# Optimization experiments

Measured on AMD Instinct MI355X. Metric: run time of the kernel, lower is better.

## Reference

```python
import jax, jax.numpy as jnp
import numpy as np

N_NODES = 20000
D = 512
H = 8
DK = D // H  # 64
L = 2


def _layernorm(x, g, b, eps=1e-5):
    mu = x.mean(-1, keepdims=True)
    var = x.var(-1, keepdims=True)
    return (x - mu) / jnp.sqrt(var + eps) * g + b


def _hgt_layer(h, kw, kb, qw, qb, vw, vb, aw, ab, pri, att_r, msg_r, skip, ln_g, ln_b, src, dst):
    # h: [N, D]
    N = h.shape[0]
    k = (h @ kw.T + kb).reshape(N, H, DK)
    q = (h @ qw.T + qb).reshape(N, H, DK)
    v = (h @ vw.T + vb).reshape(N, H, DK)
    # per-relation bilinear transforms on keys and messages
    k = jnp.einsum('nhi,hij->nhj', k, att_r)
    v = jnp.einsum('nhi,hij->nhj', v, msg_r)
    # per-edge attention scores [E, H]
    t = jnp.einsum('ehd,ehd->eh', k[src], q[dst]) * pri / jnp.sqrt(jnp.float32(DK))
    # edge softmax over incoming edges of each destination node
    mx = jax.ops.segment_max(t, dst, num_segments=N)
    e = jnp.exp(t - mx[dst])
    den = jax.ops.segment_sum(e, dst, num_segments=N)
    att = e / jnp.maximum(den[dst], 1e-9)
    # weighted message aggregation [N, H, DK] -> [N, D]
    msg = v[src] * att[..., None]
    agg = jax.ops.segment_sum(msg, dst, num_segments=N).reshape(N, D)
    trans = jax.nn.gelu(agg) @ aw.T + ab
    alpha = jax.nn.sigmoid(skip)
    out = trans * alpha + h * (1.0 - alpha)
    return _layernorm(out, ln_g, ln_b)


def setup_inputs() -> dict:
    key = jax.random.key(0)
    ks = jax.random.split(key, 16)
    B, E = 8192, 320000
    s = 0.02
    inp = {
        'embeddings': jax.random.normal(ks[0], (B, D), jnp.float32),
        'node_emb': jax.random.normal(ks[1], (N_NODES, D), jnp.float32) * s,
        'adapt_w': jax.random.normal(ks[2], (D, D), jnp.float32) * s,
        'adapt_b': jnp.zeros((D,), jnp.float32),
        'kw': jax.random.normal(ks[3], (L, D, D), jnp.float32) * s,
        'kb': jnp.zeros((L, D), jnp.float32),
        'qw': jax.random.normal(ks[4], (L, D, D), jnp.float32) * s,
        'qb': jnp.zeros((L, D), jnp.float32),
        'vw': jax.random.normal(ks[5], (L, D, D), jnp.float32) * s,
        'vb': jnp.zeros((L, D), jnp.float32),
        'aw': jax.random.normal(ks[6], (L, D, D), jnp.float32) * s,
        'ab': jnp.zeros((L, D), jnp.float32),
        'pri': jnp.ones((L, H), jnp.float32),
        'att_r': jax.random.normal(ks[7], (L, H, DK, DK), jnp.float32) * (1.0 / np.sqrt(DK)),
        'msg_r': jax.random.normal(ks[8], (L, H, DK, DK), jnp.float32) * (1.0 / np.sqrt(DK)),
        'skip': jnp.ones((L,), jnp.float32),
        'ln_g': jnp.ones((L, D), jnp.float32),
        'ln_b': jnp.zeros((L, D), jnp.float32),
        'out_w': jax.random.normal(ks[9], (D, D), jnp.float32) * s,
        'out_b': jnp.zeros((D,), jnp.float32),
        'attn_kernels': jax.random.uniform(ks[10], (D,), jnp.float32),
        'src': jax.random.randint(ks[11], (E,), 0, N_NODES, jnp.int32),
        'dst': jax.random.randint(ks[12], (E,), 0, N_NODES, jnp.int32),
        'n_classes': 10000,
    }
    return inp


def reference(embeddings, node_emb, adapt_w, adapt_b, kw, kb, qw, qb, vw, vb, aw, ab,
              pri, att_r, msg_r, skip, ln_g, ln_b, out_w, out_b, attn_kernels,
              src, dst, n_classes):
    # Hgt encoder over the label graph (single ntype '_N')
    h = jax.nn.gelu(node_emb @ adapt_w.T + adapt_b)
    for l in range(L):
        h = _hgt_layer(h, kw[l], kb[l], qw[l], qb[l], vw[l], vb[l], aw[l], ab[l],
                       pri[l], att_r[l], msg_r[l], skip[l], ln_g[l], ln_b[l], src, dst)
    cls_emb = h @ out_w.T + out_b          # [N, D]
    cls_emb = cls_emb[:n_classes]          # [C, D]  (dropout is identity in eval)
    # logits[b,c] = sum_d embeddings[b,d] * attn_kernels[d] * cls_emb[c,d]
    logits = (embeddings * attn_kernels) @ cls_emb.T
    return logits
```

## Files before the change

kernel.cpp:

```cpp
#include <hip/hip_runtime.h>
#include <hip/hip_bf16.h>

#define D 512
#define H 8
#define NLAYER 2

typedef __attribute__((ext_vector_type(8))) short short8;
typedef __attribute__((ext_vector_type(4))) short short4v;
typedef __attribute__((ext_vector_type(4))) float f32x4;

__device__ __forceinline__ float gelu_f(float x) {
    float x3 = x * x * x;
    return 0.5f * x * (1.0f + tanhf(0.7978845608028654f * (x + 0.044715f * x3)));
}

__device__ __forceinline__ unsigned short f2b(float x) {
    unsigned u = __float_as_uint(x);
    u += 0x7FFF + ((u >> 16) & 1);
    return (unsigned short)(u >> 16);
}
__device__ __forceinline__ float b2f(unsigned short u) {
    return __uint_as_float(((unsigned)u) << 16);
}

__device__ __forceinline__ void gld16(const short* g, short* l) {
    __builtin_amdgcn_global_load_lds(
        (const __attribute__((address_space(1))) void*)g,
        (__attribute__((address_space(3))) void*)l, 16, 0, 0);
}

template <int POSTG, int OUTMODE>
__global__ __launch_bounds__(256) void gemm_bf(
    const short* __restrict__ A, const short* __restrict__ B,
    const float* __restrict__ bias, float* __restrict__ Cf,
    short* __restrict__ Cb, int M, int N, int K) {
    __shared__ __align__(16) short As[2][4096];
    __shared__ __align__(16) short Bs[2][4096];
    const unsigned gx = gridDim.x, gy = gridDim.y;
    const unsigned nwg = gx * gy;
    const unsigned orig = blockIdx.y * gx + blockIdx.x;
    const unsigned q = nwg >> 3, r = nwg & 7;
    const unsigned xcd = orig & 7, sidx = orig >> 3;
    const unsigned swz = (xcd < r ? xcd * (q + 1) : r * (q + 1) + (xcd - r) * q) + sidx;
    const unsigned CH = 8;
    const unsigned chunk = swz / (CH * gx);
    const unsigned rem = swz - chunk * (CH * gx);
    const unsigned nr = min(CH, gy - chunk * CH);
    const unsigned col = rem / nr;
    const unsigned rowin = rem - col * nr;
    const int bm = (int)(chunk * CH + rowin) * 128;
    const int bn = (int)col * 128;

    const int tid = threadIdx.x;
    const int lane = tid & 63;
    const int wave = tid >> 6;
    const int wm = (wave >> 1) * 64, wn = (wave & 1) * 64;
    const int lr16 = lane & 15;
    const int lk8 = (lane >> 4) * 8;

    const int trow = tid >> 2;
    const int tchk = (tid & 3) * 8;
    const short* a0 = A + (size_t)min(bm + trow, M - 1) * K + tchk;
    const short* a1 = A + (size_t)min(bm + 64 + trow, M - 1) * K + tchk;
    const short* b0 = B + (size_t)min(bn + trow, N - 1) * K + tchk;
    const short* b1 = B + (size_t)min(bn + 64 + trow, N - 1) * K + tchk;

    auto stage = [&](int buf, int k0) {
        gld16(a0 + k0, &As[buf][tid * 8]);
        gld16(a1 + k0, &As[buf][2048 + tid * 8]);
        gld16(b0 + k0, &Bs[buf][tid * 8]);
        gld16(b1 + k0, &Bs[buf][2048 + tid * 8]);
    };

    f32x4 acc[4][4];
#pragma unroll
    for (int i = 0; i < 4; ++i)
#pragma unroll
        for (int j = 0; j < 4; ++j) acc[i][j] = (f32x4){0.f, 0.f, 0.f, 0.f};

    stage(0, 0);
    int cur = 0;
    for (int k0 = 0; k0 < K; k0 += 32) {
        __syncthreads();
        if (k0 + 32 < K) stage(cur ^ 1, k0 + 32);

        short8 af[4], bfr[4];
#pragma unroll
        for (int mi = 0; mi < 4; ++mi)
            af[mi] = *(const short8*)&As[cur][(wm + mi * 16 + lr16) * 32 + lk8];
#pragma unroll
        for (int ni = 0; ni < 4; ++ni)
            bfr[ni] = *(const short8*)&Bs[cur][(wn + ni * 16 + lr16) * 32 + lk8];
#pragma unroll
        for (int mi = 0; mi < 4; ++mi)
#pragma unroll
            for (int ni = 0; ni < 4; ++ni)
                acc[mi][ni] = __builtin_amdgcn_mfma_f32_16x16x32_bf16(
                    af[mi], bfr[ni], acc[mi][ni], 0, 0, 0);
        cur ^= 1;
    }

#pragma unroll
    for (int mi = 0; mi < 4; ++mi) {
        int row0 = bm + wm + mi * 16 + (lane >> 4) * 4;
#pragma unroll
        for (int ni = 0; ni < 4; ++ni) {
            int col2 = bn + wn + ni * 16 + lr16;
            if (col2 < N) {
                float bsv = bias ? bias[col2] : 0.0f;
#pragma unroll
                for (int rr2 = 0; rr2 < 4; ++rr2) {
                    int row = row0 + rr2;
                    if (row < M) {
                        float v = acc[mi][ni][rr2] + bsv;
                        if (POSTG) v = gelu_f(v);
                        if (OUTMODE != 1) Cf[(size_t)row * N + col2] = v;
                        if (OUTMODE != 0) Cb[(size_t)row * N + col2] = (short)f2b(v);
                    }
                }
            }
        }
    }
}

__global__ void cvt_b16(const float* __restrict__ in, short* __restrict__ out, int n8) {
    int i = blockIdx.x * 256 + threadIdx.x;
    if (i >= n8) return;
    float4 a = ((const float4*)in)[i * 2];
    float4 b = ((const float4*)in)[i * 2 + 1];
    short8 o;
    o[0] = f2b(a.x); o[1] = f2b(a.y); o[2] = f2b(a.z); o[3] = f2b(a.w);
    o[4] = f2b(b.x); o[5] = f2b(b.y); o[6] = f2b(b.z); o[7] = f2b(b.w);
    *(short8*)(out + (size_t)i * 8) = o;
}

__global__ void cp_f32(const float* __restrict__ in, float* __restrict__ out, int n) {
    int i = blockIdx.x * 256 + threadIdx.x;
    if (i < n) out[i] = in[i];
}

__global__ __launch_bounds__(256) void fuse_w(
    const float* __restrict__ w, const float* __restrict__ bsrc,
    const float* __restrict__ r, short* __restrict__ fw, float* __restrict__ fb) {
    int h = blockIdx.y;
    int dc = blockIdx.x * 64;
    __shared__ float rs[64][64];
    int tid = threadIdx.x;
    for (int i = tid; i < 4096; i += 256) rs[i >> 6][i & 63] = r[h * 4096 + i];
    __syncthreads();
    for (int rep = 0; rep < 16; ++rep) {
        int o = rep * 256 + tid;
        int j = o >> 6;
        int dd = o & 63;
        float s = 0.0f;
#pragma unroll 8
        for (int i = 0; i < 64; ++i)
            s = fmaf(rs[i][j], w[(size_t)(h * 64 + i) * D + dc + dd], s);
        fw[(size_t)(h * 64 + j) * D + dc + dd] = (short)f2b(s);
    }
    if (blockIdx.x == 0 && tid < 64) {
        float s = 0.0f;
        for (int i = 0; i < 64; ++i) s += bsrc[h * 64 + i] * rs[i][tid];
        fb[h * 64 + tid] = s;
    }
}

__global__ void zero_int(int* __restrict__ p, int n) {
    int i = blockIdx.x * 256 + threadIdx.x;
    if (i < n) p[i] = 0;
}

__global__ void hist_dst(const int* __restrict__ dst, int* __restrict__ cnt, int E) {
    int i = blockIdx.x * 256 + threadIdx.x;
    if (i < E) atomicAdd(&cnt[dst[i]], 1);
}

__global__ __launch_bounds__(1024) void scan_counts(
    const int* __restrict__ cnt, int* __restrict__ offs, int* __restrict__ cursor,
    int n, int E) {
    __shared__ int part[1024];
    int t = threadIdx.x;
    int chunk = (n + 1023) >> 10;
    int lo = t * chunk;
    int hi = min(lo + chunk, n);
    int s = 0;
    for (int i = lo; i < hi; ++i) s += cnt[i];
    part[t] = s;
    __syncthreads();
    for (int off = 1; off < 1024; off <<= 1) {
        int v = (t >= off) ? part[t - off] : 0;
        __syncthreads();
        part[t] += v;
        __syncthreads();
    }
    int base = (t == 0) ? 0 : part[t - 1];
    for (int i = lo; i < hi; ++i) {
        offs[i] = base;
        cursor[i] = base;
        base += cnt[i];
    }
    if (t == 1023) offs[n] = E;
}

__global__ void scatter_edges(const int* __restrict__ src, const int* __restrict__ dst,
                              int* __restrict__ cursor, int* __restrict__ srcs, int E) {
    int i = blockIdx.x * 256 + threadIdx.x;
    if (i < E) {
        int pos = atomicAdd(&cursor[dst[i]], 1);
        srcs[pos] = src[i];
    }
}

__global__ __launch_bounds__(256) void edge_attn(
    const short* __restrict__ kqv, const int* __restrict__ srcs,
    const int* __restrict__ offs, const float* __restrict__ pri,
    short* __restrict__ gg, int NNodes) {
    int n = blockIdx.x * 4 + (threadIdx.x >> 6);
    if (n >= NNodes) return;
    int lane = threadIdx.x & 63;
    int start = offs[n], end = offs[n + 1];

    const short8 qv = *(const short8*)(kqv + (size_t)n * 1536 + 512 + lane * 8);
    float qf[8];
#pragma unroll
    for (int j = 0; j < 8; ++j) qf[j] = b2f((unsigned short)qv[j]);
    const float prih = pri[lane >> 3] * 0.125f;

    float rm0 = -INFINITY, rd0 = 0.0f, rm1 = -INFINITY, rd1 = 0.0f;
    float va0[8], va1[8];
#pragma unroll
    for (int j = 0; j < 8; ++j) { va0[j] = 0.0f; va1[j] = 0.0f; }

    int i = start;
    for (; i + 1 < end; i += 2) {
        int s0 = srcs[i], s1 = srcs[i + 1];
        const short* r0 = kqv + (size_t)s0 * 1536;
        const short* r1 = kqv + (size_t)s1 * 1536;
        short8 k0 = *(const short8*)(r0 + lane * 8);
        short8 v0 = *(const short8*)(r0 + 1024 + lane * 8);
        short8 k1 = *(const short8*)(r1 + lane * 8);
        short8 v1 = *(const short8*)(r1 + 1024 + lane * 8);
        float d0 = 0.0f, d1 = 0.0f;
#pragma unroll
        for (int j = 0; j < 8; ++j) {
            d0 = fmaf(b2f((unsigned short)k0[j]), qf[j], d0);
            d1 = fmaf(b2f((unsigned short)k1[j]), qf[j], d1);
        }
        d0 += __shfl_xor(d0, 1); d1 += __shfl_xor(d1, 1);
        d0 += __shfl_xor(d0, 2); d1 += __shfl_xor(d1, 2);
        d0 += __shfl_xor(d0, 4); d1 += __shfl_xor(d1, 4);
        float t0 = d0 * prih, t1 = d1 * prih;
        float nm0 = fmaxf(rm0, t0), nm1 = fmaxf(rm1, t1);
        float sc0 = expf(rm0 - nm0), sc1 = expf(rm1 - nm1);
        float e0 = expf(t0 - nm0), e1 = expf(t1 - nm1);
        rd0 = rd0 * sc0 + e0; rm0 = nm0;
        rd1 = rd1 * sc1 + e1; rm1 = nm1;
#pragma unroll
        for (int j = 0; j < 8; ++j) {
            va0[j] = fmaf(va0[j], sc0, b2f((unsigned short)v0[j]) * e0);
            va1[j] = fmaf(va1[j], sc1, b2f((unsigned short)v1[j]) * e1);
        }
    }
    if (i < end) {
        int s0 = srcs[i];
        const short* r0 = kqv + (size_t)s0 * 1536;
        short8 k0 = *(const short8*)(r0 + lane * 8);
        short8 v0 = *(const short8*)(r0 + 1024 + lane * 8);
        float d0 = 0.0f;
#pragma unroll
        for (int j = 0; j < 8; ++j) d0 = fmaf(b2f((unsigned short)k0[j]), qf[j], d0);
        d0 += __shfl_xor(d0, 1);
        d0 += __shfl_xor(d0, 2);
        d0 += __shfl_xor(d0, 4);
        float t0 = d0 * prih;
        float nm0 = fmaxf(rm0, t0);
        float sc0 = expf(rm0 - nm0);
        float e0 = expf(t0 - nm0);
        rd0 = rd0 * sc0 + e0; rm0 = nm0;
#pragma unroll
        for (int j = 0; j < 8; ++j)
            va0[j] = fmaf(va0[j], sc0, b2f((unsigned short)v0[j]) * e0);
    }

    float m = fmaxf(fmaxf(rm0, rm1), -3.0e38f);
    float s0 = expf(rm0 - m), s1 = expf(rm1 - m);
    float rden = rd0 * s0 + rd1 * s1;
    float inv = 1.0f / fmaxf(rden, 1e-9f);
    unsigned o[4];
#pragma unroll
    for (int p = 0; p < 4; ++p) {
        float x0 = gelu_f((va0[2 * p] * s0 + va1[2 * p] * s1) * inv);
        float x1 = gelu_f((va0[2 * p + 1] * s0 + va1[2 * p + 1] * s1) * inv);
        o[p] = (unsigned)(unsigned short)f2b(x0) |
               ((unsigned)(unsigned short)f2b(x1) << 16);
    }
    uint4 pack = make_uint4(o[0], o[1], o[2], o[3]);
    *(uint4*)(gg + (size_t)n * D + lane * 8) = pack;
}

__global__ __launch_bounds__(128) void blend_ln(
    const float* __restrict__ trans, const float* __restrict__ hin,
    const float* __restrict__ skip, const float* __restrict__ g,
    const float* __restrict__ b, float* __restrict__ hout,
    short* __restrict__ hb16) {
    int n = blockIdx.x;
    int tid = threadIdx.x;
    float alpha = 1.0f / (1.0f + expf(-skip[0]));
    size_t base = (size_t)n * D + tid * 4;
    float4 t4 = *(const float4*)(trans + base);
    float4 h4 = *(const float4*)(hin + base);
    float o[4];
    o[0] = t4.x * alpha + h4.x * (1.0f - alpha);
    o[1] = t4.y * alpha + h4.y * (1.0f - alpha);
    o[2] = t4.z * alpha + h4.z * (1.0f - alpha);
    o[3] = t4.w * alpha + h4.w * (1.0f - alpha);
    float s = o[0] + o[1] + o[2] + o[3];
    float ss = o[0] * o[0] + o[1] * o[1] + o[2] * o[2] + o[3] * o[3];
    for (int off = 32; off; off >>= 1) {
        s += __shfl_down(s, off);
        ss += __shfl_down(ss, off);
    }
    __shared__ float red[4];
    if ((tid & 63) == 0) { red[tid >> 6] = s; red[2 + (tid >> 6)] = ss; }
    __syncthreads();
    float S = red[0] + red[1];
    float SS = red[2] + red[3];
    float mu = S * (1.0f / 512.0f);
    float var = SS * (1.0f / 512.0f) - mu * mu;
    float inv = rsqrtf(var + 1e-5f);
    int c = tid * 4;
    float4 o4;
    o4.x = (o[0] - mu) * inv * g[c + 0] + b[c + 0];
    o4.y = (o[1] - mu) * inv * g[c + 1] + b[c + 1];
    o4.z = (o[2] - mu) * inv * g[c + 2] + b[c + 2];
    o4.w = (o[3] - mu) * inv * g[c + 3] + b[c + 3];
    *(float4*)(hout + base) = o4;
    short4v hb;
    hb[0] = f2b(o4.x); hb[1] = f2b(o4.y); hb[2] = f2b(o4.z); hb[3] = f2b(o4.w);
    *(short4v*)(hb16 + base) = hb;
}

__global__ void scale_emb_b16(const float* __restrict__ e, const float* __restrict__ ak,
                              short* __restrict__ o, int n8) {
    int i = blockIdx.x * 256 + threadIdx.x;
    if (i >= n8) return;
    float4 a = ((const float4*)e)[i * 2];
    float4 b = ((const float4*)e)[i * 2 + 1];
    int d0 = (i * 8) & (D - 1);
    short8 v;
    v[0] = f2b(a.x * ak[d0 + 0]); v[1] = f2b(a.y * ak[d0 + 1]);
    v[2] = f2b(a.z * ak[d0 + 2]); v[3] = f2b(a.w * ak[d0 + 3]);
    v[4] = f2b(b.x * ak[d0 + 4]); v[5] = f2b(b.y * ak[d0 + 5]);
    v[6] = f2b(b.z * ak[d0 + 6]); v[7] = f2b(b.w * ak[d0 + 7]);
    *(short8*)(o + (size_t)i * 8) = v;
}

extern "C" void kernel_launch(void* const* d_in, const int* in_sizes, int n_in,
                              void* d_out, int out_size, void* d_ws, size_t ws_size,
                              hipStream_t stream) {
    const float* embeddings = (const float*)d_in[0];
    const float* node_emb   = (const float*)d_in[1];
    const float* adapt_w    = (const float*)d_in[2];
    const float* adapt_b    = (const float*)d_in[3];
    const float* kw   = (const float*)d_in[4];
    const float* kb   = (const float*)d_in[5];
    const float* qw   = (const float*)d_in[6];
    const float* qb   = (const float*)d_in[7];
    const float* vw   = (const float*)d_in[8];
    const float* vb   = (const float*)d_in[9];
    const float* aw   = (const float*)d_in[10];
    const float* ab   = (const float*)d_in[11];
    const float* pri  = (const float*)d_in[12];
    const float* att_r = (const float*)d_in[13];
    const float* msg_r = (const float*)d_in[14];
    const float* skip  = (const float*)d_in[15];
    const float* ln_g  = (const float*)d_in[16];
    const float* ln_b  = (const float*)d_in[17];
    const float* out_w = (const float*)d_in[18];
    const float* out_b = (const float*)d_in[19];
    const float* attn_k = (const float*)d_in[20];
    const int* src = (const int*)d_in[21];
    const int* dst = (const int*)d_in[22];

    const int E  = in_sizes[21];
    const int NB = in_sizes[0] / D;
    const int NN = in_sizes[1] / D;
    const int NC = out_size / NB;

    size_t big = (size_t)NN * D;
    float* hbuf = (float*)d_ws;
    float* fb32 = hbuf + big;
    short* hb16 = (short*)(fb32 + big);
    short* gg16 = hb16 + big;
    short* kqv16 = gg16 + big;
    short* w16a = kqv16 + (size_t)NN * 1536;
    short* w16o = w16a + (size_t)D * D;
    short* w16w = w16o + (size_t)D * D;
    short* wcat = w16w + (size_t)D * D;
    float* bcat = (float*)(wcat + (size_t)1536 * D);
    int* offs   = (int*)(bcat + 1536);
    int* cursor = offs + NN + 1;
    int* srcs   = cursor + NN;
    short* cls16 = kqv16;
    short* embs16 = kqv16 + (size_t)NC * D;

    auto ggrid = [](int M, int N) { return dim3((N + 127) / 128, (M + 127) / 128); };
    const int WB = D * D / 8;

    zero_int<<<(NN + 255) / 256, 256, 0, stream>>>(cursor, NN);
    hist_dst<<<(E + 255) / 256, 256, 0, stream>>>(dst, cursor, E);
    scan_counts<<<1, 1024, 0, stream>>>(cursor, offs, cursor, NN, E);
    scatter_edges<<<(E + 255) / 256, 256, 0, stream>>>(src, dst, cursor, srcs, E);

    cvt_b16<<<((int)(big / 8) + 255) / 256, 256, 0, stream>>>(node_emb, gg16, (int)(big / 8));
    cvt_b16<<<(WB + 255) / 256, 256, 0, stream>>>(adapt_w, w16a, WB);
    cvt_b16<<<(WB + 255) / 256, 256, 0, stream>>>(out_w, w16o, WB);

    gemm_bf<1, 2><<<ggrid(NN, D), 256, 0, stream>>>(gg16, w16a, adapt_b, hbuf, hb16, NN, D, D);

    for (int l = 0; l < NLAYER; ++l) {
        const size_t wo = (size_t)l * D * D;
        fuse_w<<<dim3(8, 8), 256, 0, stream>>>(kw + wo, kb + l * D, att_r + (size_t)l * H * 64 * 64, wcat, bcat);
        cvt_b16<<<(WB + 255) / 256, 256, 0, stream>>>(qw + wo, wcat + (size_t)512 * D, WB);
        cp_f32<<<2, 256, 0, stream>>>(qb + l * D, bcat + 512, D);
        fuse_w<<<dim3(8, 8), 256, 0, stream>>>(vw + wo, vb + l * D, msg_r + (size_t)l * H * 64 * 64, wcat + (size_t)1024 * D, bcat + 1024);

        gemm_bf<0, 1><<<ggrid(NN, 1536), 256, 0, stream>>>(hb16, wcat, bcat, nullptr, kqv16, NN, 1536, D);

        edge_attn<<<(NN + 3) / 4, 256, 0, stream>>>(kqv16, srcs, offs, pri + l * H, gg16, NN);

        cvt_b16<<<(WB + 255) / 256, 256, 0, stream>>>(aw + wo, w16w, WB);
        gemm_bf<0, 0><<<ggrid(NN, D), 256, 0, stream>>>(gg16, w16w, ab + l * D, fb32, nullptr, NN, D, D);
        blend_ln<<<NN, 128, 0, stream>>>(fb32, hbuf, skip + l, ln_g + l * D, ln_b + l * D, hbuf, hb16);
    }

    gemm_bf<0, 1><<<ggrid(NC, D), 256, 0, stream>>>(hb16, w16o, out_b, nullptr, cls16, NC, D, D);
    scale_emb_b16<<<((NB * D / 8) + 255) / 256, 256, 0, stream>>>(embeddings, attn_k, embs16, NB * D / 8);
    gemm_bf<0, 0><<<ggrid(NB, NC), 256, 0, stream>>>(embs16, cls16, nullptr, (float*)d_out, nullptr, NB, NC, D);
}
```

Before: 861.8 us.

## Deepen GEMM prefetch to two stages and merge per-layer weight prep kernels

The bf16 GEMM main loop now issues global-to-LDS loads two k-steps ahead. It waits on explicit vmcnt counts and uses split barriers so the next stage's loads overlap the MFMA work instead of following a full syncthreads. Separately, the per-layer weight fusion, q/a weight conversion and bias copy are folded into one prep_layer launch, which replaces five launches per layer. The hand-written waitcnt values depend on each thread issuing exactly four loads per stage, so the code is fragile if the staging changes.

```diff
diff --git a/kernel.cpp b/kernel.cpp
--- a/kernel.cpp
+++ b/kernel.cpp
@@ -79,10 +79,15 @@
         for (int j = 0; j < 4; ++j) acc[i][j] = (f32x4){0.f, 0.f, 0.f, 0.f};
 
     stage(0, 0);
+    stage(1, 32);
     int cur = 0;
     for (int k0 = 0; k0 < K; k0 += 32) {
-        __syncthreads();
-        if (k0 + 32 < K) stage(cur ^ 1, k0 + 32);
+        if (k0 + 32 < K) {
+            asm volatile("s_waitcnt vmcnt(4)" ::: "memory");
+        } else {
+            asm volatile("s_waitcnt vmcnt(0)" ::: "memory");
+        }
+        __builtin_amdgcn_s_barrier();
 
         short8 af[4], bfr[4];
 #pragma unroll
@@ -91,6 +96,12 @@
 #pragma unroll
         for (int ni = 0; ni < 4; ++ni)
             bfr[ni] = *(const short8*)&Bs[cur][(wn + ni * 16 + lr16) * 32 + lk8];
+        asm volatile("s_waitcnt lgkmcnt(0)" ::: "memory");
+        __builtin_amdgcn_sched_barrier(0);
+        __builtin_amdgcn_s_barrier();
+
+        if (k0 + 64 < K) stage(cur, k0 + 64);
+
 #pragma unroll
         for (int mi = 0; mi < 4; ++mi)
 #pragma unroll
@@ -134,34 +145,58 @@
     *(short8*)(out + (size_t)i * 8) = o;
 }
 
-__global__ void cp_f32(const float* __restrict__ in, float* __restrict__ out, int n) {
-    int i = blockIdx.x * 256 + threadIdx.x;
-    if (i < n) out[i] = in[i];
-}
-
-__global__ __launch_bounds__(256) void fuse_w(
-    const float* __restrict__ w, const float* __restrict__ bsrc,
-    const float* __restrict__ r, short* __restrict__ fw, float* __restrict__ fb) {
-    int h = blockIdx.y;
-    int dc = blockIdx.x * 64;
+__global__ __launch_bounds__(256) void prep_layer(
+    const float* __restrict__ kw, const float* __restrict__ kb,
+    const float* __restrict__ qw, const float* __restrict__ qb,
+    const float* __restrict__ vw, const float* __restrict__ vb,
+    const float* __restrict__ aw,
+    const float* __restrict__ att_r, const float* __restrict__ msg_r,
+    short* __restrict__ wcat, float* __restrict__ bcat,
+    short* __restrict__ w16w) {
     __shared__ float rs[64][64];
+    int bid = blockIdx.x;
     int tid = threadIdx.x;
-    for (int i = tid; i < 4096; i += 256) rs[i >> 6][i & 63] = r[h * 4096 + i];
-    __syncthreads();
-    for (int rep = 0; rep < 16; ++rep) {
-        int o = rep * 256 + tid;
-        int j = o >> 6;
-        int dd = o & 63;
-        float s = 0.0f;
+    if (bid < 128) {
+        int which = bid >> 6;
+        int sub = bid & 63;
+        int h = sub >> 3, dc = (sub & 7) * 64;
+        const float* w = which ? vw : kw;
+        const float* bsrc = which ? vb : kb;
+        const float* rr = (which ? msg_r : att_r) + h * 4096;
+        short* fw = wcat + (which ? (size_t)1024 * D : 0);
+        float* fb = bcat + (which ? 1024 : 0);
+        for (int i = tid; i < 4096; i += 256) rs[i >> 6][i & 63] = rr[i];
+        __syncthreads();
+        for (int rep = 0; rep < 16; ++rep) {
+            int o = rep * 256 + tid;
+            int j = o >> 6;
+            int dd = o & 63;
+            float s = 0.0f;
 #pragma unroll 8
-        for (int i = 0; i < 64; ++i)
-            s = fmaf(rs[i][j], w[(size_t)(h * 64 + i) * D + dc + dd], s);
-        fw[(size_t)(h * 64 + j) * D + dc + dd] = (short)f2b(s);
-    }
-    if (blockIdx.x == 0 && tid < 64) {
-        float s = 0.0f;
-        for (int i = 0; i < 64; ++i) s += bsrc[h * 64 + i] * rs[i][tid];
-        fb[h * 64 + tid] = s;
+            for (int i = 0; i < 64; ++i)
+                s = fmaf(rs[i][j], w[(size_t)(h * 64 + i) * D + dc + dd], s);
+            fw[(size_t)(h * 64 + j) * D + dc + dd] = (short)f2b(s);
+        }
+        if ((sub & 7) == 0 && tid < 64) {
+            float s = 0.0f;
+            for (int i = 0; i < 64; ++i) s += bsrc[h * 64 + i] * rs[i][tid];
+            fb[h * 64 + tid] = s;
+        }
+    } else if (bid < 384) {
+        int cb = bid - 128;
+        const float* in = qw;
+        short* out = wcat + (size_t)512 * D;
+        if (cb >= 128) { in = aw; out = w16w; cb -= 128; }
+        int i = cb * 256 + tid;
+        float4 a = ((const float4*)in)[i * 2];
+        float4 b = ((const float4*)in)[i * 2 + 1];
+        short8 o;
+        o[0] = f2b(a.x); o[1] = f2b(a.y); o[2] = f2b(a.z); o[3] = f2b(a.w);
+        o[4] = f2b(b.x); o[5] = f2b(b.y); o[6] = f2b(b.z); o[7] = f2b(b.w);
+        *(short8*)(out + (size_t)i * 8) = o;
+    } else {
+        bcat[512 + tid * 2] = qb[tid * 2];
+        bcat[512 + tid * 2 + 1] = qb[tid * 2 + 1];
     }
 }
 
@@ -420,16 +455,15 @@
 
     for (int l = 0; l < NLAYER; ++l) {
         const size_t wo = (size_t)l * D * D;
-        fuse_w<<<dim3(8, 8), 256, 0, stream>>>(kw + wo, kb + l * D, att_r + (size_t)l * H * 64 * 64, wcat, bcat);
-        cvt_b16<<<(WB + 255) / 256, 256, 0, stream>>>(qw + wo, wcat + (size_t)512 * D, WB);
-        cp_f32<<<2, 256, 0, stream>>>(qb + l * D, bcat + 512, D);
-        fuse_w<<<dim3(8, 8), 256, 0, stream>>>(vw + wo, vb + l * D, msg_r + (size_t)l * H * 64 * 64, wcat + (size_t)1024 * D, bcat + 1024);
+        prep_layer<<<385, 256, 0, stream>>>(
+            kw + wo, kb + l * D, qw + wo, qb + l * D, vw + wo, vb + l * D,
+            aw + wo, att_r + (size_t)l * H * 64 * 64, msg_r + (size_t)l * H * 64 * 64,
+            wcat, bcat, w16w);
 
         gemm_bf<0, 1><<<ggrid(NN, 1536), 256, 0, stream>>>(hb16, wcat, bcat, nullptr, kqv16, NN, 1536, D);
 
         edge_attn<<<(NN + 3) / 4, 256, 0, stream>>>(kqv16, srcs, offs, pri + l * H, gg16, NN);
 
-        cvt_b16<<<(WB + 255) / 256, 256, 0, stream>>>(aw + wo, w16w, WB);
         gemm_bf<0, 0><<<ggrid(NN, D), 256, 0, stream>>>(gg16, w16w, ab + l * D, fb32, nullptr, NN, D, D);
         blend_ln<<<NN, 128, 0, stream>>>(fb32, hbuf, skip + l, ln_g + l * D, ln_b + l * D, hbuf, hb16);
     }
```

Result: faster. 782.9 us (-9.2%).
